# Optimization experiments

Hardware: AMD Instinct MI355X
Metric: run time of the kernel (lower is better)

Reference implementation:

```python
import jax, jax.numpy as jnp
import numpy as np

NUM_HEADS = 16
NUM_KV_HEADS = 4
HEAD_DIM = 256
ROPE_THETA = 10000.0


def _rope(x, position_ids):
    # x: [B, H, S, D], position_ids: [B, S]
    d = x.shape[-1]
    inv_freq = 1.0 / (ROPE_THETA ** (jnp.arange(0, d, 2, dtype=jnp.float32) / d))  # [D/2]
    freqs = position_ids.astype(jnp.float32)[:, :, None] * inv_freq[None, None, :]  # [B, S, D/2]
    emb = jnp.concatenate([freqs, freqs], axis=-1)  # [B, S, D]
    cos = jnp.cos(emb)[:, None, :, :]
    sin = jnp.sin(emb)[:, None, :, :]
    x1, x2 = jnp.split(x, 2, axis=-1)
    rot = jnp.concatenate([-x2, x1], axis=-1)
    return x * cos + rot * sin


def setup_inputs() -> dict:
    key = jax.random.key(0)
    k1, k2, k3, k4, k5 = jax.random.split(key, 5)
    B, S, H = 2, 2048, 2048
    hidden_states = jax.random.normal(k1, (B, S, H), dtype=jnp.float32)
    position_ids = jnp.broadcast_to(jnp.arange(S, dtype=jnp.int32)[None, :], (B, S))
    scale = 1.0 / np.sqrt(H)
    wq = jax.random.normal(k2, (H, NUM_HEADS * HEAD_DIM), dtype=jnp.float32) * scale
    wk = jax.random.normal(k3, (H, NUM_KV_HEADS * HEAD_DIM), dtype=jnp.float32) * scale
    wv = jax.random.normal(k4, (H, NUM_KV_HEADS * HEAD_DIM), dtype=jnp.float32) * scale
    wo = jax.random.normal(k5, (NUM_HEADS * HEAD_DIM, H), dtype=jnp.float32) * (1.0 / np.sqrt(NUM_HEADS * HEAD_DIM))
    return {"hidden_states": hidden_states, "position_ids": position_ids,
            "wq": wq, "wk": wk, "wv": wv, "wo": wo}


def reference(hidden_states, position_ids, wq, wk, wv, wo):
    B, S, H = hidden_states.shape
    groups = NUM_HEADS // NUM_KV_HEADS
    # QKV projections -> [B, heads, S, D]
    q = (hidden_states @ wq).reshape(B, S, NUM_HEADS, HEAD_DIM).transpose(0, 2, 1, 3)
    k = (hidden_states @ wk).reshape(B, S, NUM_KV_HEADS, HEAD_DIM).transpose(0, 2, 1, 3)
    v = (hidden_states @ wv).reshape(B, S, NUM_KV_HEADS, HEAD_DIM).transpose(0, 2, 1, 3)
    q = _rope(q, position_ids)
    k = _rope(k, position_ids)
    # GQA without materializing repeated K/V: group query heads per kv head
    qg = q.reshape(B, NUM_KV_HEADS, groups, S, HEAD_DIM)
    scale = 1.0 / jnp.sqrt(jnp.asarray(HEAD_DIM, dtype=q.dtype))
    scores = jnp.einsum('bkgqd,bkvd->bkgqv', qg, k) * scale  # [B, KV, G, S, S]
    causal = jnp.tril(jnp.ones((S, S), dtype=bool))
    scores = jnp.where(causal[None, None, None, :, :], scores, jnp.finfo(scores.dtype).min)
    probs = jax.nn.softmax(scores, axis=-1)
    out = jnp.einsum('bkgqv,bkvd->bkgqd', probs, v)  # [B, KV, G, S, D]
    out = out.reshape(B, NUM_HEADS, S, HEAD_DIM).transpose(0, 2, 1, 3).reshape(B, S, NUM_HEADS * HEAD_DIM)
    return out @ wo
```

## Files before the change

kernel.cpp:

```cpp
#include <hip/hip_runtime.h>

typedef unsigned short u16;
typedef __bf16 bf16_t;
typedef bf16_t bf16x8 __attribute__((ext_vector_type(8)));
typedef float f32x4 __attribute__((ext_vector_type(4)));
typedef float f32x16 __attribute__((ext_vector_type(16)));

#define LOG2E 1.4426950408889634f
#define QKVS 6144

__device__ __forceinline__ u16 f2bf(float f) {
  union { float f; unsigned u; } c; c.f = f;
  unsigned r = c.u + 0x7fffu + ((c.u >> 16) & 1u);
  return (u16)(r >> 16);
}
__device__ __forceinline__ float bf2f(u16 u) {
  union { unsigned u; float f; } c; c.u = ((unsigned)u) << 16;
  return c.f;
}

__device__ __forceinline__ void gload16(const void* g, void* l) {
  __builtin_amdgcn_global_load_lds(
      (const __attribute__((address_space(1))) unsigned int*)g,
      (__attribute__((address_space(3))) unsigned int*)l, 16, 0, 0);
}

__device__ __forceinline__ unsigned cvtpk(float lo, float hi) {
  unsigned r;
  asm("v_cvt_pk_bf16_f32 %0, %1, %2" : "=v"(r) : "v"(lo), "v"(hi));
  return r;
}
__device__ __forceinline__ void swap32(unsigned& a, unsigned& b) {
  asm("v_permlane32_swap_b32 %0, %1" : "+v"(a), "+v"(b));
}

#define MFMA16(a, b, c) __builtin_amdgcn_mfma_f32_16x16x32_bf16((a), (b), (c), 0, 0, 0)
#define MFMA32(a, b, c) __builtin_amdgcn_mfma_f32_32x32x16_bf16((a), (b), (c), 0, 0, 0)


__global__ __launch_bounds__(256) void k_convert_f32_bf16(const float* __restrict__ in,
                                                          u16* __restrict__ out, int n4) {
  int i = blockIdx.x * 256 + threadIdx.x;
  if (i >= n4) return;
  float4 v = ((const float4*)in)[i];
  ushort4 o;
  o.x = f2bf(v.x); o.y = f2bf(v.y); o.z = f2bf(v.z); o.w = f2bf(v.w);
  ((ushort4*)out)[i] = o;
}

__global__ __launch_bounds__(256) void k_transpose_f32_bf16(const float* __restrict__ in,
                                                            u16* __restrict__ out, int R, int C) {
  __shared__ float tile[32][33];
  int tx = threadIdx.x, ty = threadIdx.y;
  int bx = blockIdx.x * 32, by = blockIdx.y * 32;
#pragma unroll
  for (int i = 0; i < 4; i++)
    tile[ty + i * 8][tx] = in[(size_t)(by + ty + i * 8) * C + bx + tx];
  __syncthreads();
#pragma unroll
  for (int i = 0; i < 4; i++)
    out[(size_t)(bx + ty + i * 8) * R + by + tx] = f2bf(tile[tx][ty + i * 8]);
}

__global__ __launch_bounds__(256) void k_transpose_bf16(const u16* __restrict__ in,
                                                        u16* __restrict__ out, int R, int C) {
  __shared__ u16 tile[32][33];
  int tx = threadIdx.x, ty = threadIdx.y;
  int bx = blockIdx.x * 32, by = blockIdx.y * 32;
#pragma unroll
  for (int i = 0; i < 4; i++)
    tile[ty + i * 8][tx] = in[(size_t)(by + ty + i * 8) * C + bx + tx];
  __syncthreads();
#pragma unroll
  for (int i = 0; i < 4; i++)
    out[(size_t)(bx + ty + i * 8) * R + by + tx] = tile[tx][ty + i * 8];
}

__global__ __launch_bounds__(256) void k_ropetab(const int* __restrict__ pos,
                                                 float2* __restrict__ tab) {
  int idx = blockIdx.x * 256 + threadIdx.x;
  int i = idx & 127, row = idx >> 7;
  float p = (float)pos[row];
  float f = p * exp2f((float)i * (-13.287712379549449f / 128.f));
  float sn, cs;
  sincosf(f, &sn, &cs);
  tab[idx] = make_float2(cs, sn);
}

__global__ __launch_bounds__(256) void k_ropeqk(u16* __restrict__ x,
                                                const float2* __restrict__ tab) {
  int idx = blockIdx.x * 256 + threadIdx.x;
  int i = idx & 127;
  int rh = idx >> 7;
  int row = rh / 20;
  int h = rh - row * 20;
  float2 t = tab[row * 128 + i];
  size_t base = (size_t)row * QKVS + h * 256 + i;
  float x1 = bf2f(x[base]), x2 = bf2f(x[base + 128]);
  x[base] = f2bf(x1 * t.x - x2 * t.y);
  x[base + 128] = f2bf(x2 * t.x + x1 * t.y);
}


template <int OUT_BF16>
__global__ __launch_bounds__(256) void k_gemm_bt(const u16* __restrict__ A,
                                                 const u16* __restrict__ Bt,
                                                 void* __restrict__ C, int M, int N, int K) {
  __shared__ u16 As[128 * 64];
  __shared__ u16 Bs[128 * 64];
  const int tid = threadIdx.x;
  const int lane = tid & 63;
  const int w = tid >> 6;
  const int l15 = lane & 15, l4 = lane >> 4;
  const int wr = w >> 1, wc = w & 1;
  const int bx = blockIdx.x, by = blockIdx.y;

  f32x4 acc[4][4];
#pragma unroll
  for (int a = 0; a < 4; a++)
#pragma unroll
    for (int b2 = 0; b2 < 4; b2++) acc[a][b2] = (f32x4){0.f, 0.f, 0.f, 0.f};

  const u16* Abase = A + (size_t)by * 128 * K;
  const u16* Bbase = Bt + (size_t)bx * 128 * K;

  for (int kk = 0; kk < K; kk += 64) {
    __syncthreads();
#pragma unroll
    for (int j = 0; j < 4; j++) {
      int ci = w * 256 + j * 64 + lane;
      int row = ci >> 3, c = ci & 7;
      gload16(Abase + (size_t)row * K + kk + c * 8, (char*)As + ci * 16);
      gload16(Bbase + (size_t)row * K + kk + c * 8, (char*)Bs + ci * 16);
    }
    __syncthreads();
#pragma unroll
    for (int kc = 0; kc < 2; kc++) {
      int kb = kc * 64 + l4 * 16;
      bf16x8 av[4], bv[4];
#pragma unroll
      for (int mt = 0; mt < 4; mt++)
        av[mt] = *(const bf16x8*)((const char*)As + (wr * 64 + mt * 16 + l15) * 128 + kb);
#pragma unroll
      for (int nt = 0; nt < 4; nt++)
        bv[nt] = *(const bf16x8*)((const char*)Bs + (wc * 64 + nt * 16 + l15) * 128 + kb);
#pragma unroll
      for (int mt = 0; mt < 4; mt++)
#pragma unroll
        for (int nt = 0; nt < 4; nt++) acc[mt][nt] = MFMA16(av[mt], bv[nt], acc[mt][nt]);
    }
  }
#pragma unroll
  for (int mt = 0; mt < 4; mt++) {
#pragma unroll
    for (int nt = 0; nt < 4; nt++) {
      int col = bx * 128 + wc * 64 + nt * 16 + l15;
#pragma unroll
      for (int r = 0; r < 4; r++) {
        int row = by * 128 + wr * 64 + mt * 16 + l4 * 4 + r;
        if (OUT_BF16)
          ((u16*)C)[(size_t)row * N + col] = f2bf(acc[mt][nt][r]);
        else
          ((float*)C)[(size_t)row * N + col] = acc[mt][nt][r];
      }
    }
  }
}


__global__ __launch_bounds__(512, 1) void k_gemm256(const u16* __restrict__ A,
                                                    const u16* __restrict__ Bt,
                                                    u16* __restrict__ C, int N, int K) {
  extern __shared__ char smem[];
  const int tid = threadIdx.x;
  const int lane = tid & 63, w = tid >> 6;
  const int l15 = lane & 15, l4 = lane >> 4;
  const int wr = w >> 2, wc = w & 3;
  const int bx = blockIdx.x, by = blockIdx.y;
  const int NT = K >> 6;

  const u16* Ab = A + (size_t)(by * 256) * K;
  const u16* Bb = Bt + (size_t)(bx * 256) * K;

  int srcoff[2], dstoff[2];
#pragma unroll
  for (int rr = 0; rr < 2; rr++) {
    int ci = rr * 512 + tid;
    int lc = ci ^ (((ci >> 5) & 1) << 1);
    int kc = lc >> 9, row = (lc >> 2) & 127, g2 = lc & 3;
    srcoff[rr] = row * K + kc * 32 + g2 * 8;
    dstoff[rr] = ci * 16;
  }

  auto SH = [&](int Tg, int halfidx) {
    const u16* base = (halfidx < 2) ? (Ab + (size_t)(halfidx * 128) * K)
                                    : (Bb + (size_t)((halfidx - 2) * 128) * K);
    char* dst = smem + (Tg & 1) * 65536 + halfidx * 16384;
    int kk = Tg * 64;
#pragma unroll
    for (int rr = 0; rr < 2; rr++)
      gload16(base + srcoff[rr] + kk, dst + dstoff[rr]);
  };

  auto lda = [&](int c, int kc, int mrow4) -> bf16x8 {
    int L = kc * 8192 + (mrow4 * 16 + l15) * 64 + l4 * 16;
    int P = L ^ (((L >> 9) & 1) << 5);
    return *(const bf16x8*)(smem + c * 65536 + wr * 16384 + P);
  };
  auto ldb = [&](int c, int kc, int j) -> bf16x8 {
    int L = kc * 8192 + ((wc & 1) * 64 + j * 16 + l15) * 64 + l4 * 16;
    int P = L ^ (((L >> 9) & 1) << 5);
    return *(const bf16x8*)(smem + c * 65536 + 32768 + (wc >> 1) * 16384 + P);
  };

  f32x4 acc[8][4];
#pragma unroll
  for (int i = 0; i < 8; i++)
#pragma unroll
    for (int j = 0; j < 4; j++) acc[i][j] = (f32x4){0.f, 0.f, 0.f, 0.f};

  SH(0, 0); SH(0, 1); SH(0, 2); SH(0, 3);
  SH(1, 2); SH(1, 3);
  asm volatile("s_waitcnt vmcnt(4)" ::: "memory");
  __builtin_amdgcn_s_barrier();
  asm volatile("" ::: "memory");

  bf16x8 bv[2][4];
  for (int T = 0; T < NT; ++T) {
    const int c = T & 1;
#pragma unroll
    for (int q = 0; q < 4; q++) {
      const int kc = q & 1, mh = q >> 1;
      bf16x8 av[4];
      if (q < 2) {
#pragma unroll
        for (int j = 0; j < 4; j++) bv[kc][j] = ldb(c, kc, j);
      }
#pragma unroll
      for (int ii = 0; ii < 4; ii++) av[ii] = lda(c, kc, mh * 4 + ii);
      if (q == 0)      { if (T + 1 < NT) SH(T + 1, 0); }
      else if (q == 1) { if (T + 1 < NT) SH(T + 1, 1); }
      else if (q == 2) { if (T + 2 < NT) SH(T + 2, 2); }
      else             { if (T + 2 < NT) SH(T + 2, 3); }
      if (q == 3) {
        if (T < NT - 2)       asm volatile("s_waitcnt vmcnt(4)" ::: "memory");
        else if (T == NT - 2) asm volatile("s_waitcnt vmcnt(0)" ::: "memory");
      }
      asm volatile("" ::: "memory");
      __builtin_amdgcn_s_barrier();
      asm volatile("" ::: "memory");
      asm volatile("s_waitcnt lgkmcnt(0)" ::: "memory");
      __builtin_amdgcn_sched_barrier(0);
      __builtin_amdgcn_s_setprio(1);
#pragma unroll
      for (int ii = 0; ii < 4; ii++)
#pragma unroll
        for (int j = 0; j < 4; j++)
          acc[mh * 4 + ii][j] = MFMA16(av[ii], bv[kc][j], acc[mh * 4 + ii][j]);
      __builtin_amdgcn_s_setprio(0);
      asm volatile("" ::: "memory");
      __builtin_amdgcn_s_barrier();
      asm volatile("" ::: "memory");
    }
  }

#pragma unroll
  for (int i = 0; i < 8; i++) {
#pragma unroll
    for (int j = 0; j < 4; j++) {
      int col = bx * 256 + wc * 64 + j * 16 + l15;
#pragma unroll
      for (int r = 0; r < 4; r++) {
        int row = by * 256 + wr * 128 + i * 16 + l4 * 4 + r;
        C[(size_t)row * N + col] = f2bf(acc[i][j][r]);
      }
    }
  }
}


__shared__ __align__(16) u16 aK0[8192];
__shared__ __align__(16) u16 aK1[8192];
__shared__ __align__(16) u16 aV0[8192];
__shared__ __align__(16) u16 aV1[8192];

__global__ __launch_bounds__(256, 2) void k_attn(const u16* __restrict__ QKV,
                                                 const u16* __restrict__ Vt,
                                                 u16* __restrict__ AO) {
  const int tid = threadIdx.x, lane = tid & 63, w = tid >> 6;
  const int r31 = lane & 31, hi = lane >> 5;

  const int flat = blockIdx.x;
  const int r = flat & 7;
  const int idx = flat >> 3;
  const int b = r >> 2, kv = r & 3;
  const int half = idx >> 5, j = idx & 31;
  const int qb = half ? 15 - (j >> 1) : (j >> 1);
  const int h = kv * 4 + (j & 1) + 2 * half;

  bf16x8 qreg[16];
  {
    const u16* qp = QKV + (size_t)(b * 2048 + qb * 128 + w * 32 + r31) * QKVS + h * 256 + hi * 8;
#pragma unroll
    for (int kc = 0; kc < 16; kc++) qreg[kc] = *(const bf16x8*)(qp + kc * 16);
  }

  f32x16 o[8];
#pragma unroll
  for (int df = 0; df < 8; df++)
#pragma unroll
    for (int jj = 0; jj < 16; jj++) o[df][jj] = 0.f;
  float mrow = -3e38f, lrow = 0.f;

  const int nt = 4 * qb + 4;
  const int tlim = 4 * qb + w;
  const int qloc = qb * 128 + w * 32 + r31;
  const u16* Kbase = QKV + (size_t)(b * 2048) * QKVS + 4096 + kv * 256;
  const u16* Vbase = Vt + (size_t)(kv * 256) * 4096 + b * 2048;

  int kfix[4], vfix[4];
#pragma unroll
  for (int jj = 0; jj < 4; jj++) {
    int ci = jj * 256 + tid;
    int krow = ci >> 5, kc = ci & 31;
    int kcg = (kc & 24) | ((kc ^ krow) & 7);
    kfix[jj] = krow * QKVS + kcg * 8;
    int vrow = ci >> 2, vc = ci & 3;
    int vg = (vc - (vrow >> 1)) & 3;
    vfix[jj] = vrow * 4096 + vg * 8;
  }
  int koff = 0, voff = 0;

  auto STAGE = [&](u16* Kd, u16* Vd) {
#pragma unroll
    for (int jj = 0; jj < 4; jj++)
      gload16(Kbase + kfix[jj] + koff, (char*)Kd + (jj * 256 + tid) * 16);
#pragma unroll
    for (int jj = 0; jj < 4; jj++)
      gload16(Vbase + vfix[jj] + voff, (char*)Vd + (jj * 256 + tid) * 16);
    koff += 32 * QKVS;
    voff += 32;
  };

  auto COMPUTE = [&](int t, const u16* Kc, const u16* Vc) {
    f32x16 s;
#pragma unroll
    for (int jj = 0; jj < 16; jj++) s[jj] = 0.f;
#pragma unroll
    for (int kc = 0; kc < 16; kc++) {
      int ch = kc * 2 + hi;
      int cs = (ch & 24) | ((ch ^ r31) & 7);
      bf16x8 kf = *(const bf16x8*)((const char*)Kc + r31 * 512 + cs * 16);
      s = MFMA32(kf, qreg[kc], s);
    }

    const float C = 0.0625f * LOG2E;
    float z[16];
#pragma unroll
    for (int jj = 0; jj < 16; jj++) z[jj] = s[jj] * C;
    if (t == tlim) {
#pragma unroll
      for (int jj = 0; jj < 16; jj++) {
        int kvg = t * 32 + (jj & 3) + 8 * (jj >> 2) + 4 * hi;
        if (kvg > qloc) z[jj] = -1e30f;
      }
    }

    float m0 = z[0];
#pragma unroll
    for (int jj = 1; jj < 16; jj++) m0 = fmaxf(m0, z[jj]);
    m0 = fmaxf(m0, __shfl_xor(m0, 32));
    if (__any(m0 > mrow + 11.54f)) {
      float mn = fmaxf(mrow, m0);
      float alpha = exp2f(mrow - mn);
      mrow = mn;
      lrow *= alpha;
#pragma unroll
      for (int jj = 0; jj < 16; jj++) {
        float a = __shfl(alpha, (jj & 3) + 8 * (jj >> 2) + 4 * hi);
#pragma unroll
        for (int df = 0; df < 8; df++) o[df][jj] *= a;
      }
    }
    float sum = 0.f;
#pragma unroll
    for (int jj = 0; jj < 16; jj++) {
      z[jj] = exp2f(z[jj] - mrow);
      sum += z[jj];
    }
    sum += __shfl_xor(sum, 32);
    lrow += sum;

    unsigned a0 = cvtpk(z[0], z[1]), a2 = cvtpk(z[4], z[5]);
    swap32(a0, a2);
    unsigned a1 = cvtpk(z[2], z[3]), a3 = cvtpk(z[6], z[7]);
    swap32(a1, a3);
    unsigned b0 = cvtpk(z[8], z[9]), b2 = cvtpk(z[12], z[13]);
    swap32(b0, b2);
    unsigned b1 = cvtpk(z[10], z[11]), b3 = cvtpk(z[14], z[15]);
    swap32(b1, b3);
    union UU { unsigned u[4]; bf16x8 v; };
    UU ua; ua.u[0] = a0; ua.u[1] = a1; ua.u[2] = a2; ua.u[3] = a3;
    UU ub; ub.u[0] = b0; ub.u[1] = b1; ub.u[2] = b2; ub.u[3] = b3;
    bf16x8 pa0 = ua.v, pa1 = ub.v;

#pragma unroll
    for (int df = 0; df < 8; df++) {
      int vr = df * 32 + r31;
      int c0 = (hi + (vr >> 1)) & 3;
      int c1 = (2 + hi + (vr >> 1)) & 3;
      bf16x8 v0 = *(const bf16x8*)((const char*)Vc + vr * 64 + c0 * 16);
      bf16x8 v1 = *(const bf16x8*)((const char*)Vc + vr * 64 + c1 * 16);
      o[df] = MFMA32(pa0, v0, o[df]);
      o[df] = MFMA32(pa1, v1, o[df]);
    }
  };

  STAGE(aK0, aV0);
  __syncthreads();

  for (int t = 0; t < nt; t += 2) {
    STAGE(aK1, aV1);
    if (t <= tlim) COMPUTE(t, aK0, aV0);
    __syncthreads();
    if (t + 2 < nt) STAGE(aK0, aV0);
    if (t + 1 <= tlim) COMPUTE(t + 1, aK1, aV1);
    __syncthreads();
  }

  float rl = 1.f / lrow;
  size_t rowbase = (size_t)(b * 2048 + qb * 128 + w * 32);
#pragma unroll
  for (int jj = 0; jj < 16; jj++) {
    float rr2 = __shfl(rl, (jj & 3) + 8 * (jj >> 2) + 4 * hi);
    int qr = (jj & 3) + 8 * (jj >> 2) + 4 * hi;
#pragma unroll
    for (int df = 0; df < 8; df++)
      AO[(rowbase + qr) * 4096 + h * 256 + df * 32 + r31] = f2bf(o[df][jj] * rr2);
  }
}


#define OFF_AO    0u
#define OFF_XB    0u
#define OFF_WQKVT 16777216u
#define OFF_VT    33554432u
#define OFF_WOT   41943040u
#define OFF_QKV   58720256u
#define OFF_TAB   109051904u

extern "C" void kernel_launch(void* const* d_in, const int* in_sizes, int n_in,
                              void* d_out, int out_size, void* d_ws, size_t ws_size,
                              hipStream_t stream) {
  const float* hs = (const float*)d_in[0];
  const int* pos = (const int*)d_in[1];
  const float* wq = (const float*)d_in[2];
  const float* wk = (const float*)d_in[3];
  const float* wv = (const float*)d_in[4];
  const float* wo = (const float*)d_in[5];
  float* out = (float*)d_out;
  char* ws = (char*)d_ws;

  u16* Xb    = (u16*)(ws + OFF_XB);
  u16* Wqkvt = (u16*)(ws + OFF_WQKVT);
  u16* Vt    = (u16*)(ws + OFF_VT);
  u16* Wot   = (u16*)(ws + OFF_WOT);
  u16* QKV   = (u16*)(ws + OFF_QKV);
  float2* Tab = (float2*)(ws + OFF_TAB);
  u16* AO    = (u16*)(ws + OFF_AO);

  dim3 tb(32, 8);

  k_ropetab<<<2048, 256, 0, stream>>>(pos, Tab);

  k_convert_f32_bf16<<<8192, 256, 0, stream>>>(hs, Xb, 2097152);
  k_transpose_f32_bf16<<<dim3(128, 64), tb, 0, stream>>>(wq, Wqkvt, 2048, 4096);
  k_transpose_f32_bf16<<<dim3(32, 64), tb, 0, stream>>>(wk, Wqkvt + 4096 * 2048, 2048, 1024);
  k_transpose_f32_bf16<<<dim3(32, 64), tb, 0, stream>>>(wv, Wqkvt + 5120 * 2048, 2048, 1024);
  k_transpose_f32_bf16<<<dim3(64, 128), tb, 0, stream>>>(wo, Wot, 4096, 2048);

  (void)hipFuncSetAttribute((const void*)k_gemm256,
                            hipFuncAttributeMaxDynamicSharedMemorySize, 131072);
  k_gemm256<<<dim3(24, 16), 512, 131072, stream>>>(Xb, Wqkvt, QKV, 6144, 2048);

  k_ropeqk<<<40960, 256, 0, stream>>>(QKV, Tab);

  k_transpose_bf16<<<dim3(32, 128), tb, 0, stream>>>(QKV + 5120, Vt, 4096, QKVS);

  k_attn<<<dim3(512), 256, 0, stream>>>(QKV, Vt, AO);

  k_gemm_bt<0><<<dim3(16, 32), 256, 0, stream>>>(AO, Wot, out, 4096, 2048, 4096);
}
```

Before: 473.7 us.

## Fuse RoPE into QKV GEMM epilogue and merge weight transposes into one launch

```diff
diff --git a/kernel.cpp b/kernel.cpp
--- a/kernel.cpp
+++ b/kernel.cpp
@@ -48,11 +48,32 @@
   ((ushort4*)out)[i] = o;
 }
 
-__global__ __launch_bounds__(256) void k_transpose_f32_bf16(const float* __restrict__ in,
-                                                            u16* __restrict__ out, int R, int C) {
+__global__ __launch_bounds__(256) void k_transpose_all(const float* __restrict__ wq,
+                                                       const float* __restrict__ wk,
+                                                       const float* __restrict__ wv,
+                                                       const float* __restrict__ wo,
+                                                       u16* __restrict__ Wqkvt,
+                                                       u16* __restrict__ Wot) {
   __shared__ float tile[32][33];
-  int tx = threadIdx.x, ty = threadIdx.y;
-  int bx = blockIdx.x * 32, by = blockIdx.y * 32;
+  int fb = blockIdx.x;
+  const float* in;
+  u16* out;
+  int R, C, bxi, byi;
+  if (fb < 8192) {
+    in = wq; out = Wqkvt; R = 2048; C = 4096;
+    bxi = fb & 127; byi = fb >> 7;
+  } else if (fb < 10240) {
+    in = wk; out = Wqkvt + 4096 * 2048; R = 2048; C = 1024;
+    int l = fb - 8192; bxi = l & 31; byi = l >> 5;
+  } else if (fb < 12288) {
+    in = wv; out = Wqkvt + 5120 * 2048; R = 2048; C = 1024;
+    int l = fb - 10240; bxi = l & 31; byi = l >> 5;
+  } else {
+    in = wo; out = Wot; R = 4096; C = 2048;
+    int l = fb - 12288; bxi = l & 63; byi = l >> 6;
+  }
+  int tx = threadIdx.x & 31, ty = threadIdx.x >> 5;
+  int bx = bxi * 32, by = byi * 32;
 #pragma unroll
   for (int i = 0; i < 4; i++)
     tile[ty + i * 8][tx] = in[(size_t)(by + ty + i * 8) * C + bx + tx];
@@ -85,20 +106,6 @@
   float sn, cs;
   sincosf(f, &sn, &cs);
   tab[idx] = make_float2(cs, sn);
-}
-
-__global__ __launch_bounds__(256) void k_ropeqk(u16* __restrict__ x,
-                                                const float2* __restrict__ tab) {
-  int idx = blockIdx.x * 256 + threadIdx.x;
-  int i = idx & 127;
-  int rh = idx >> 7;
-  int row = rh / 20;
-  int h = rh - row * 20;
-  float2 t = tab[row * 128 + i];
-  size_t base = (size_t)row * QKVS + h * 256 + i;
-  float x1 = bf2f(x[base]), x2 = bf2f(x[base + 128]);
-  x[base] = f2bf(x1 * t.x - x2 * t.y);
-  x[base + 128] = f2bf(x2 * t.x + x1 * t.y);
 }
 
 
@@ -170,7 +177,8 @@
 
 __global__ __launch_bounds__(512, 1) void k_gemm256(const u16* __restrict__ A,
                                                     const u16* __restrict__ Bt,
-                                                    u16* __restrict__ C, int N, int K) {
+                                                    u16* __restrict__ C, int N, int K,
+                                                    const float2* __restrict__ tab) {
   extern __shared__ char smem[];
   const int tid = threadIdx.x;
   const int lane = tid & 63, w = tid >> 6;
@@ -264,15 +272,49 @@
     }
   }
 
-#pragma unroll
-  for (int i = 0; i < 8; i++) {
-#pragma unroll
-    for (int j = 0; j < 4; j++) {
-      int col = bx * 256 + wc * 64 + j * 16 + l15;
-#pragma unroll
-      for (int r = 0; r < 4; r++) {
-        int row = by * 256 + wr * 128 + i * 16 + l4 * 4 + r;
-        C[(size_t)row * N + col] = f2bf(acc[i][j][r]);
+  if (bx < 20) {
+    float* X = (float*)smem;
+    const float sgn = (wc < 2) ? -1.f : 1.f;
+    const int ptid = tid ^ 128;
+#pragma unroll
+    for (int ih = 0; ih < 2; ih++) {
+      __syncthreads();
+#pragma unroll
+      for (int i2 = 0; i2 < 4; i2++)
+#pragma unroll
+        for (int j2 = 0; j2 < 4; j2++)
+#pragma unroll
+          for (int r2 = 0; r2 < 4; r2++)
+            X[tid * 64 + i2 * 16 + j2 * 4 + r2] = acc[ih * 4 + i2][j2][r2];
+      __syncthreads();
+#pragma unroll
+      for (int i2 = 0; i2 < 4; i2++) {
+#pragma unroll
+        for (int j2 = 0; j2 < 4; j2++) {
+          int col = bx * 256 + wc * 64 + j2 * 16 + l15;
+          int ti = (wc & 1) * 64 + j2 * 16 + l15;
+#pragma unroll
+          for (int r2 = 0; r2 < 4; r2++) {
+            int row = by * 256 + wr * 128 + (ih * 4 + i2) * 16 + l4 * 4 + r2;
+            float mine = acc[ih * 4 + i2][j2][r2];
+            float part = X[ptid * 64 + i2 * 16 + j2 * 4 + r2];
+            float2 t = tab[(size_t)row * 128 + ti];
+            C[(size_t)row * N + col] = f2bf(mine * t.x + sgn * part * t.y);
+          }
+        }
+      }
+    }
+  } else {
+#pragma unroll
+    for (int i = 0; i < 8; i++) {
+#pragma unroll
+      for (int j = 0; j < 4; j++) {
+        int col = bx * 256 + wc * 64 + j * 16 + l15;
+#pragma unroll
+        for (int r = 0; r < 4; r++) {
+          int row = by * 256 + wr * 128 + i * 16 + l4 * 4 + r;
+          C[(size_t)row * N + col] = f2bf(acc[i][j][r]);
+        }
       }
     }
   }
@@ -474,16 +516,11 @@
   k_ropetab<<<2048, 256, 0, stream>>>(pos, Tab);
 
   k_convert_f32_bf16<<<8192, 256, 0, stream>>>(hs, Xb, 2097152);
-  k_transpose_f32_bf16<<<dim3(128, 64), tb, 0, stream>>>(wq, Wqkvt, 2048, 4096);
-  k_transpose_f32_bf16<<<dim3(32, 64), tb, 0, stream>>>(wk, Wqkvt + 4096 * 2048, 2048, 1024);
-  k_transpose_f32_bf16<<<dim3(32, 64), tb, 0, stream>>>(wv, Wqkvt + 5120 * 2048, 2048, 1024);
-  k_transpose_f32_bf16<<<dim3(64, 128), tb, 0, stream>>>(wo, Wot, 4096, 2048);
+  k_transpose_all<<<20480, 256, 0, stream>>>(wq, wk, wv, wo, Wqkvt, Wot);
 
   (void)hipFuncSetAttribute((const void*)k_gemm256,
                             hipFuncAttributeMaxDynamicSharedMemorySize, 131072);
-  k_gemm256<<<dim3(24, 16), 512, 131072, stream>>>(Xb, Wqkvt, QKV, 6144, 2048);
-
-  k_ropeqk<<<40960, 256, 0, stream>>>(QKV, Tab);
+  k_gemm256<<<dim3(24, 16), 512, 131072, stream>>>(Xb, Wqkvt, QKV, 6144, 2048, Tab);
 
   k_transpose_bf16<<<dim3(32, 128), tb, 0, stream>>>(QKV + 5120, Vt, 4096, QKVS);
 
```

Result: slower. 553.1 us (+16.8%).
